# Kernel tuning notes

Hardware: AMD Instinct MI355X
Metric: run time of the kernel (lower is better)

The kernel has to match this reference:

```python
import jax, jax.numpy as jnp
import numpy as np

D_MODEL = 1024


def setup_inputs() -> dict:
    key = jax.random.key(0)
    ks = jax.random.split(key, 7)
    d = D_MODEL
    x = jax.random.normal(ks[0], (4, 2048, d), dtype=jnp.float32)
    scale = 1.0 / np.sqrt(d)
    Wq = jax.random.normal(ks[1], (d, d), dtype=jnp.float32) * scale
    bq = jax.random.normal(ks[2], (d,), dtype=jnp.float32) * 0.01
    Wk = jax.random.normal(ks[3], (d, d), dtype=jnp.float32) * scale
    bk = jax.random.normal(ks[4], (d,), dtype=jnp.float32) * 0.01
    Wo = jax.random.normal(ks[5], (d, 1), dtype=jnp.float32) * scale
    bo = jax.random.normal(ks[6], (1,), dtype=jnp.float32) * 0.01
    return {"x": x, "Wq": Wq, "bq": bq, "Wk": Wk, "bk": bk, "Wo": Wo, "bo": bo}


def reference(x, Wq, bq, Wk, bk, Wo, bo):
    # x: [B, N, d]
    Q = x @ Wq + bq                      # [B, N, d]
    K = x @ Wk + bk                      # [B, N, d]
    scale = x.shape[-1] ** (-0.5)
    content_logits = jnp.einsum('bnd,bmd->bnm', Q, K) * scale  # [B, N, N]
    s = (x @ Wo + bo)[..., 0]            # [B, N]
    # ordering_bias[b, i, j] = tanh(s[b, j] - s[b, i]) * 5
    ordering_bias = jnp.tanh(s[:, None, :] - s[:, :, None]) * 5.0
    return content_logits + ordering_bias
```

## Files before the change

kernel.cpp:

```cpp
#include <hip/hip_runtime.h>
#include <math.h>

#define D_MODEL 1024
#define SEQ 2048
#define SCALE 0.03125f

using bf16x8 = __attribute__((ext_vector_type(8))) short;
using f32x4  = __attribute__((ext_vector_type(4))) float;

__device__ __forceinline__ unsigned short f2bf(float f) {
  union { float f; unsigned int u; } v; v.f = f;
  return (unsigned short)((v.u + 0x7fffu + ((v.u >> 16) & 1u)) >> 16);
}

__device__ __forceinline__ void async_cp16(const void* g, void* l) {
  __builtin_amdgcn_global_load_lds(
      (const __attribute__((address_space(1))) void*)g,
      (__attribute__((address_space(3))) void*)l, 16, 0, 0);
}


__device__ __forceinline__ const unsigned short* sptr(
    const unsigned short* base, int row0, int t) {
  const int rr = t >> 3;
  const int ck = (t & 7) ^ (rr & 7);
  return base + (size_t)(row0 + rr) * D_MODEL + ck * 8;
}

#define STG8(KT, BUF) {                                                    \
    const unsigned short* a_ = sA + (KT) * 64;                             \
    const unsigned short* b_ = sB + (KT) * 64;                             \
    unsigned short* da_ = As + (BUF) * 8192 + t * 8;                       \
    unsigned short* db_ = Bs + (BUF) * 8192 + t * 8;                       \
    async_cp16(a_,                 da_);                                   \
    async_cp16(a_ + 32 * D_MODEL,  da_ + 2048);                            \
    async_cp16(a_ + 64 * D_MODEL,  da_ + 4096);                            \
    async_cp16(a_ + 96 * D_MODEL,  da_ + 6144);                            \
    async_cp16(b_,                 db_);                                   \
    async_cp16(b_ + 32 * D_MODEL,  db_ + 2048);                            \
    async_cp16(b_ + 64 * D_MODEL,  db_ + 4096);                            \
    async_cp16(b_ + 96 * D_MODEL,  db_ + 6144);                            \
  }

__device__ __forceinline__ void gemm128_bk64(
    const unsigned short* sA, const unsigned short* sB,
    unsigned short* As, unsigned short* Bs, int t, f32x4 acc[4][4]) {
  const int lane = t & 63, w = t >> 6;
  const int wm = w >> 1, wn = w & 1;
  const int l16 = lane & 15, quad = lane >> 4, x7 = l16 & 7;
  const int c0 = (quad ^ x7) * 8, c1 = ((4 | quad) ^ x7) * 8;

  STG8(0, 0);
  __syncthreads();

  #pragma unroll 2
  for (int kk = 0; kk < 16; ++kk) {
    const int cur = (kk & 1) * 8192;
    if (kk < 15) STG8(kk + 1, (kk & 1) ^ 1);
    bf16x8 afr[4][2], bfr[4][2];
    #pragma unroll
    for (int mt = 0; mt < 4; mt++) {
      const int base = cur + (wm * 64 + mt * 16 + l16) * 64;
      afr[mt][0] = *(const bf16x8*)(As + base + c0);
      afr[mt][1] = *(const bf16x8*)(As + base + c1);
    }
    #pragma unroll
    for (int nt = 0; nt < 4; nt++) {
      const int base = cur + (wn * 64 + nt * 16 + l16) * 64;
      bfr[nt][0] = *(const bf16x8*)(Bs + base + c0);
      bfr[nt][1] = *(const bf16x8*)(Bs + base + c1);
    }
    #pragma unroll
    for (int ks = 0; ks < 2; ks++)
      #pragma unroll
      for (int mt = 0; mt < 4; mt++)
        #pragma unroll
        for (int nt = 0; nt < 4; nt++)
          acc[mt][nt] = __builtin_amdgcn_mfma_f32_16x16x32_bf16(
              afr[mt][ks], bfr[nt][ks], acc[mt][nt], 0, 0, 0);
    __syncthreads();
  }
}

__device__ __forceinline__ void store_c_bf16(f32x4 acc[4][4],
                                             unsigned short* C, int ldc,
                                             int m0, int n0, int tid) {
  const int lane = tid & 63, w = tid >> 6;
  const int wm = w >> 1, wn = w & 1;
  const int l16 = lane & 15, quad = lane >> 4;
  #pragma unroll
  for (int mt = 0; mt < 4; mt++) {
    #pragma unroll
    for (int r = 0; r < 4; r++) {
      const int row = m0 + wm * 64 + mt * 16 + quad * 4 + r;
      unsigned short* cp = C + (size_t)row * ldc + n0 + wn * 64 + l16;
      #pragma unroll
      for (int nt = 0; nt < 4; nt++) cp[nt * 16] = f2bf(acc[mt][nt][r]);
    }
  }
}

__global__ __launch_bounds__(256) void wcvt_kernel(
    const float* __restrict__ Wq, const float* __restrict__ Wk,
    const float* __restrict__ bq, const float* __restrict__ bk,
    unsigned short* __restrict__ Wqb, unsigned short* __restrict__ Wkb,
    float* __restrict__ u, float* __restrict__ v, float* __restrict__ sc) {
  const int blk = blockIdx.x, tid = threadIdx.x;
  __shared__ float red[4];
  float p;
  if (blk < 2048) {
    const bool isq = blk < 1024;
    const int row = blk & 1023;
    const float* W = isq ? Wq : Wk;
    const float* bias = isq ? bk : bq;
    const float4 wv = ((const float4*)(W + (size_t)row * D_MODEL))[tid];
    const float4 bv = ((const float4*)bias)[tid];
    ushort4 o;
    o.x = f2bf(wv.x); o.y = f2bf(wv.y); o.z = f2bf(wv.z); o.w = f2bf(wv.w);
    ((ushort4*)((isq ? Wqb : Wkb) + (size_t)row * D_MODEL))[tid] = o;
    p = wv.x * bv.x + wv.y * bv.y + wv.z * bv.z + wv.w * bv.w;
    #pragma unroll
    for (int off = 32; off > 0; off >>= 1) p += __shfl_down(p, off, 64);
    if ((tid & 63) == 0) red[tid >> 6] = p;
    __syncthreads();
    if (tid == 0) (isq ? u : v)[row] = red[0] + red[1] + red[2] + red[3];
  } else {
    const float4 a = ((const float4*)bq)[tid];
    const float4 b = ((const float4*)bk)[tid];
    p = a.x * b.x + a.y * b.y + a.z * b.z + a.w * b.w;
    #pragma unroll
    for (int off = 32; off > 0; off >>= 1) p += __shfl_down(p, off, 64);
    if ((tid & 63) == 0) red[tid >> 6] = p;
    __syncthreads();
    if (tid == 0) sc[0] = SCALE * (red[0] + red[1] + red[2] + red[3]);
  }
}

__global__ __launch_bounds__(256) void prep_x_kernel(
    const float* __restrict__ x, const float* __restrict__ Wo,
    const float* __restrict__ bo, const float* __restrict__ u,
    const float* __restrict__ v, const float* __restrict__ sc,
    unsigned short* __restrict__ xb, float* __restrict__ tb,
    float* __restrict__ aa, float* __restrict__ bb) {
  const int m = blockIdx.x, tid = threadIdx.x;
  const float4 xv = ((const float4*)(x + (size_t)m * D_MODEL))[tid];
  const float4 wv = ((const float4*)Wo)[tid];
  const float4 uv = ((const float4*)u)[tid];
  const float4 vv = ((const float4*)v)[tid];
  ushort4 o;
  o.x = f2bf(xv.x); o.y = f2bf(xv.y); o.z = f2bf(xv.z); o.w = f2bf(xv.w);
  ((ushort4*)(xb + (size_t)m * D_MODEL))[tid] = o;
  float p0 = xv.x * wv.x + xv.y * wv.y + xv.z * wv.z + xv.w * wv.w;
  float p1 = xv.x * uv.x + xv.y * uv.y + xv.z * uv.z + xv.w * uv.w;
  float p2 = xv.x * vv.x + xv.y * vv.y + xv.z * vv.z + xv.w * vv.w;
  #pragma unroll
  for (int off = 32; off > 0; off >>= 1) {
    p0 += __shfl_down(p0, off, 64);
    p1 += __shfl_down(p1, off, 64);
    p2 += __shfl_down(p2, off, 64);
  }
  __shared__ float red[3][4];
  if ((tid & 63) == 0) {
    red[0][tid >> 6] = p0; red[1][tid >> 6] = p1; red[2][tid >> 6] = p2;
  }
  __syncthreads();
  if (tid == 0) {
    tb[m] = tanhf(red[0][0] + red[0][1] + red[0][2] + red[0][3] + bo[0]);
    aa[m] = SCALE * (red[1][0] + red[1][1] + red[1][2] + red[1][3]) + sc[0];
    bb[m] = SCALE * (red[2][0] + red[2][1] + red[2][2] + red[2][3]);
  }
}

__global__ __launch_bounds__(256, 2) void wmm_kernel(
    const unsigned short* __restrict__ Wkb,
    const unsigned short* __restrict__ Wqb, unsigned short* __restrict__ Mt) {
  const int m0 = blockIdx.x * 128, n0 = blockIdx.y * 128;
  __shared__ unsigned short As[2 * 8192], Bs[2 * 8192];
  const int t = threadIdx.x;
  f32x4 acc[4][4];
  #pragma unroll
  for (int i = 0; i < 4; i++)
    #pragma unroll
    for (int j = 0; j < 4; j++) acc[i][j] = f32x4{0.f, 0.f, 0.f, 0.f};
  gemm128_bk64(sptr(Wkb, m0, t), sptr(Wqb, n0, t), As, Bs, t, acc);
  store_c_bf16(acc, Mt, D_MODEL, m0, n0, t);
}

__global__ __launch_bounds__(256, 2) void zgen_kernel(
    const unsigned short* __restrict__ xb,
    const unsigned short* __restrict__ Mt, unsigned short* __restrict__ Zb) {
  const int m0 = blockIdx.x * 128, n0 = blockIdx.y * 128;
  __shared__ unsigned short As[2 * 8192], Bs[2 * 8192];
  const int t = threadIdx.x;
  f32x4 acc[4][4];
  #pragma unroll
  for (int i = 0; i < 4; i++)
    #pragma unroll
    for (int j = 0; j < 4; j++) acc[i][j] = f32x4{0.f, 0.f, 0.f, 0.f};
  gemm128_bk64(sptr(xb, m0, t), sptr(Mt, n0, t), As, Bs, t, acc);
  store_c_bf16(acc, Zb, D_MODEL, m0, n0, t);
}

__global__ __launch_bounds__(256, 2) void zxt_kernel(
    const unsigned short* __restrict__ Zb, const unsigned short* __restrict__ xb,
    const float* __restrict__ tb, const float* __restrict__ aa,
    const float* __restrict__ bb, float* __restrict__ out) {
  __shared__ unsigned short As[2 * 8192], Bs[2 * 8192];
  __shared__ float tsi[128], tsa[128], tsj[128], tsb2[128];
  const int n = blockIdx.z * 256 + blockIdx.y * 16 + blockIdx.x;
  const int xcd = n & 7, q = n >> 3;
  const int b = q >> 5, r = q & 31;
  const int i0 = ((xcd >> 1) * 4 + (r >> 3)) * 128;
  const int j0 = ((xcd & 1) * 8 + (r & 7)) * 128;
  const int t = threadIdx.x;

  if (t < 128) {
    tsi[t] = tb[b * SEQ + i0 + t];
    tsa[t] = aa[b * SEQ + i0 + t];
  } else {
    tsj[t - 128] = tb[b * SEQ + j0 + t - 128];
    tsb2[t - 128] = bb[b * SEQ + j0 + t - 128];
  }

  f32x4 acc[4][4];
  #pragma unroll
  for (int i = 0; i < 4; i++)
    #pragma unroll
    for (int j = 0; j < 4; j++) acc[i][j] = f32x4{0.f, 0.f, 0.f, 0.f};
  gemm128_bk64(sptr(Zb + (size_t)b * SEQ * D_MODEL, i0, t),
               sptr(xb + (size_t)b * SEQ * D_MODEL, j0, t), As, Bs, t, acc);

  const int lane = t & 63, w = t >> 6;
  const int wm = w >> 1, wn = w & 1;
  const int l16 = lane & 15, quad = lane >> 4;
  float tj[4], bj[4];
  #pragma unroll
  for (int nt = 0; nt < 4; nt++) {
    tj[nt] = tsj[wn * 64 + nt * 16 + l16];
    bj[nt] = tsb2[wn * 64 + nt * 16 + l16];
  }
  #pragma unroll
  for (int mt = 0; mt < 4; mt++) {
    #pragma unroll
    for (int rr = 0; rr < 4; rr++) {
      const int il = wm * 64 + mt * 16 + quad * 4 + rr;
      const float ti = tsi[il];
      const float ai = tsa[il];
      float* cp =
          out + ((size_t)(b * SEQ + i0 + il)) * SEQ + j0 + wn * 64 + l16;
      #pragma unroll
      for (int nt = 0; nt < 4; nt++) {
        const float num = tj[nt] - ti;
        const float den = fmaf(-tj[nt], ti, 1.0f);
        const float obias = 5.0f * num * __builtin_amdgcn_rcpf(den);
        cp[nt * 16] = SCALE * acc[mt][nt][rr] + ai + bj[nt] + obias;
      }
    }
  }
}

extern "C" void kernel_launch(void* const* d_in, const int* in_sizes, int n_in,
                              void* d_out, int out_size, void* d_ws,
                              size_t ws_size, hipStream_t stream) {
  const float* x  = (const float*)d_in[0];
  const float* Wq = (const float*)d_in[1];
  const float* bq = (const float*)d_in[2];
  const float* Wk = (const float*)d_in[3];
  const float* bk = (const float*)d_in[4];
  const float* Wo = (const float*)d_in[5];
  const float* bo = (const float*)d_in[6];
  float* out = (float*)d_out;

  char* ws = (char*)d_ws;
  unsigned short* xb  = (unsigned short*)(ws);
  unsigned short* Zb  = (unsigned short*)(ws + (16ull << 20));
  unsigned short* Wqb = (unsigned short*)(ws + (32ull << 20));
  unsigned short* Wkb = (unsigned short*)(ws + (34ull << 20));
  unsigned short* Mt  = (unsigned short*)(ws + (36ull << 20));
  float* tb = (float*)(ws + (38ull << 20));
  float* aa = (float*)(ws + (38ull << 20) + (32ull << 10));
  float* bb = (float*)(ws + (38ull << 20) + (64ull << 10));
  float* u  = (float*)(ws + (38ull << 20) + (96ull << 10));
  float* v  = (float*)(ws + (38ull << 20) + (100ull << 10));
  float* sc = (float*)(ws + (38ull << 20) + (104ull << 10));

  wcvt_kernel<<<2049, 256, 0, stream>>>(Wq, Wk, bq, bk, Wqb, Wkb, u, v, sc);
  prep_x_kernel<<<8192, 256, 0, stream>>>(x, Wo, bo, u, v, sc, xb, tb, aa, bb);
  wmm_kernel<<<dim3(8, 8), 256, 0, stream>>>(Wkb, Wqb, Mt);
  zgen_kernel<<<dim3(64, 8), 256, 0, stream>>>(xb, Mt, Zb);
  zxt_kernel<<<dim3(16, 16, 4), 256, 0, stream>>>(Zb, xb, tb, aa, bb, out);
}
```

Before: 182.7 us.

## Fuse all stages into one persistent kernel with grid-wide barriers

Replaces the five separate launches with a single persistent 512-block kernel that runs every stage and separates dependent stages with atomic-counter grid barriers. The weight-product GEMM (Wk·Wq) now overlaps with the x-conversion stage by giving those tiles to blocks 448-511 while the other blocks convert x. This removes launch gaps and tail idle time between small kernels. In exchange it depends on all 512 blocks being co-resident (two per CU), adds spin-wait barrier cost, and puts all x-conversion work on fewer blocks.

```diff
diff --git a/kernel.cpp b/kernel.cpp
--- a/kernel.cpp
+++ b/kernel.cpp
@@ -4,6 +4,7 @@
 #define D_MODEL 1024
 #define SEQ 2048
 #define SCALE 0.03125f
+#define NBLK 512u
 
 using bf16x8 = __attribute__((ext_vector_type(8))) short;
 using f32x4  = __attribute__((ext_vector_type(4))) float;
@@ -17,6 +18,20 @@
   __builtin_amdgcn_global_load_lds(
       (const __attribute__((address_space(1))) void*)g,
       (__attribute__((address_space(3))) void*)l, 16, 0, 0);
+}
+
+__device__ __forceinline__ void grid_barrier(unsigned int* cnt) {
+  __syncthreads();
+  if (threadIdx.x == 0) {
+    __threadfence();
+    __hip_atomic_fetch_add(cnt, 1u, __ATOMIC_ACQ_REL, __HIP_MEMORY_SCOPE_AGENT);
+    while (__hip_atomic_load(cnt, __ATOMIC_ACQUIRE, __HIP_MEMORY_SCOPE_AGENT) <
+           NBLK) {
+      __builtin_amdgcn_s_sleep(8);
+    }
+    __threadfence();
+  }
+  __syncthreads();
 }
 
 
@@ -100,160 +115,162 @@
   }
 }
 
-__global__ __launch_bounds__(256) void wcvt_kernel(
-    const float* __restrict__ Wq, const float* __restrict__ Wk,
-    const float* __restrict__ bq, const float* __restrict__ bk,
+__global__ __launch_bounds__(256, 2) void mega_kernel(
+    const float* __restrict__ x, const float* __restrict__ Wq,
+    const float* __restrict__ bq, const float* __restrict__ Wk,
+    const float* __restrict__ bk, const float* __restrict__ Wo,
+    const float* __restrict__ bo, float* __restrict__ out,
+    unsigned short* __restrict__ xb, unsigned short* __restrict__ Zb,
     unsigned short* __restrict__ Wqb, unsigned short* __restrict__ Wkb,
-    float* __restrict__ u, float* __restrict__ v, float* __restrict__ sc) {
-  const int blk = blockIdx.x, tid = threadIdx.x;
-  __shared__ float red[4];
-  float p;
-  if (blk < 2048) {
-    const bool isq = blk < 1024;
-    const int row = blk & 1023;
-    const float* W = isq ? Wq : Wk;
-    const float* bias = isq ? bk : bq;
-    const float4 wv = ((const float4*)(W + (size_t)row * D_MODEL))[tid];
-    const float4 bv = ((const float4*)bias)[tid];
-    ushort4 o;
-    o.x = f2bf(wv.x); o.y = f2bf(wv.y); o.z = f2bf(wv.z); o.w = f2bf(wv.w);
-    ((ushort4*)((isq ? Wqb : Wkb) + (size_t)row * D_MODEL))[tid] = o;
-    p = wv.x * bv.x + wv.y * bv.y + wv.z * bv.z + wv.w * bv.w;
-    #pragma unroll
-    for (int off = 32; off > 0; off >>= 1) p += __shfl_down(p, off, 64);
-    if ((tid & 63) == 0) red[tid >> 6] = p;
-    __syncthreads();
-    if (tid == 0) (isq ? u : v)[row] = red[0] + red[1] + red[2] + red[3];
+    unsigned short* __restrict__ Mt, float* __restrict__ tb,
+    float* __restrict__ aa, float* __restrict__ bb, float* __restrict__ u,
+    float* __restrict__ v, float* __restrict__ sc,
+    unsigned int* __restrict__ bar) {
+  __shared__ unsigned short As[2 * 8192], Bs[2 * 8192];
+  __shared__ float bias4[4][128];
+  __shared__ float red3[3][4];
+  const int blk = blockIdx.x, t = threadIdx.x;
+
+  for (int item = blk; item < 2049; item += 512) {
+    float p;
+    if (item < 2048) {
+      const bool isq = item < 1024;
+      const int row = item & 1023;
+      const float* W = isq ? Wq : Wk;
+      const float* bias = isq ? bk : bq;
+      const float4 wv = ((const float4*)(W + (size_t)row * D_MODEL))[t];
+      const float4 bv = ((const float4*)bias)[t];
+      ushort4 o;
+      o.x = f2bf(wv.x); o.y = f2bf(wv.y); o.z = f2bf(wv.z); o.w = f2bf(wv.w);
+      ((ushort4*)((isq ? Wqb : Wkb) + (size_t)row * D_MODEL))[t] = o;
+      p = wv.x * bv.x + wv.y * bv.y + wv.z * bv.z + wv.w * bv.w;
+      #pragma unroll
+      for (int off = 32; off > 0; off >>= 1) p += __shfl_down(p, off, 64);
+      if ((t & 63) == 0) red3[0][t >> 6] = p;
+      __syncthreads();
+      if (t == 0)
+        (isq ? u : v)[row] = red3[0][0] + red3[0][1] + red3[0][2] + red3[0][3];
+      __syncthreads();
+    } else {
+      const float4 a = ((const float4*)bq)[t];
+      const float4 b = ((const float4*)bk)[t];
+      p = a.x * b.x + a.y * b.y + a.z * b.z + a.w * b.w;
+      #pragma unroll
+      for (int off = 32; off > 0; off >>= 1) p += __shfl_down(p, off, 64);
+      if ((t & 63) == 0) red3[0][t >> 6] = p;
+      __syncthreads();
+      if (t == 0)
+        sc[0] = SCALE * (red3[0][0] + red3[0][1] + red3[0][2] + red3[0][3]);
+      __syncthreads();
+    }
+  }
+  grid_barrier(bar + 0);
+
+  if (blk < 448) {
+    const float4 wv = ((const float4*)Wo)[t];
+    const float4 uv = ((const float4*)u)[t];
+    const float4 vv = ((const float4*)v)[t];
+    const float scv = sc[0];
+    const float bov = bo[0];
+    for (int m = blk; m < 8192; m += 448) {
+      const float4 xv = ((const float4*)(x + (size_t)m * D_MODEL))[t];
+      ushort4 o;
+      o.x = f2bf(xv.x); o.y = f2bf(xv.y); o.z = f2bf(xv.z); o.w = f2bf(xv.w);
+      ((ushort4*)(xb + (size_t)m * D_MODEL))[t] = o;
+      float p0 = xv.x * wv.x + xv.y * wv.y + xv.z * wv.z + xv.w * wv.w;
+      float p1 = xv.x * uv.x + xv.y * uv.y + xv.z * uv.z + xv.w * uv.w;
+      float p2 = xv.x * vv.x + xv.y * vv.y + xv.z * vv.z + xv.w * vv.w;
+      #pragma unroll
+      for (int off = 32; off > 0; off >>= 1) {
+        p0 += __shfl_down(p0, off, 64);
+        p1 += __shfl_down(p1, off, 64);
+        p2 += __shfl_down(p2, off, 64);
+      }
+      if ((t & 63) == 0) {
+        red3[0][t >> 6] = p0; red3[1][t >> 6] = p1; red3[2][t >> 6] = p2;
+      }
+      __syncthreads();
+      if (t == 0) {
+        tb[m] = tanhf(red3[0][0] + red3[0][1] + red3[0][2] + red3[0][3] + bov);
+        aa[m] = SCALE * (red3[1][0] + red3[1][1] + red3[1][2] + red3[1][3]) + scv;
+        bb[m] = SCALE * (red3[2][0] + red3[2][1] + red3[2][2] + red3[2][3]);
+      }
+      __syncthreads();
+    }
   } else {
-    const float4 a = ((const float4*)bq)[tid];
-    const float4 b = ((const float4*)bk)[tid];
-    p = a.x * b.x + a.y * b.y + a.z * b.z + a.w * b.w;
-    #pragma unroll
-    for (int off = 32; off > 0; off >>= 1) p += __shfl_down(p, off, 64);
-    if ((tid & 63) == 0) red[tid >> 6] = p;
-    __syncthreads();
-    if (tid == 0) sc[0] = SCALE * (red[0] + red[1] + red[2] + red[3]);
-  }
-}
-
-__global__ __launch_bounds__(256) void prep_x_kernel(
-    const float* __restrict__ x, const float* __restrict__ Wo,
-    const float* __restrict__ bo, const float* __restrict__ u,
-    const float* __restrict__ v, const float* __restrict__ sc,
-    unsigned short* __restrict__ xb, float* __restrict__ tb,
-    float* __restrict__ aa, float* __restrict__ bb) {
-  const int m = blockIdx.x, tid = threadIdx.x;
-  const float4 xv = ((const float4*)(x + (size_t)m * D_MODEL))[tid];
-  const float4 wv = ((const float4*)Wo)[tid];
-  const float4 uv = ((const float4*)u)[tid];
-  const float4 vv = ((const float4*)v)[tid];
-  ushort4 o;
-  o.x = f2bf(xv.x); o.y = f2bf(xv.y); o.z = f2bf(xv.z); o.w = f2bf(xv.w);
-  ((ushort4*)(xb + (size_t)m * D_MODEL))[tid] = o;
-  float p0 = xv.x * wv.x + xv.y * wv.y + xv.z * wv.z + xv.w * wv.w;
-  float p1 = xv.x * uv.x + xv.y * uv.y + xv.z * uv.z + xv.w * uv.w;
-  float p2 = xv.x * vv.x + xv.y * vv.y + xv.z * vv.z + xv.w * vv.w;
-  #pragma unroll
-  for (int off = 32; off > 0; off >>= 1) {
-    p0 += __shfl_down(p0, off, 64);
-    p1 += __shfl_down(p1, off, 64);
-    p2 += __shfl_down(p2, off, 64);
-  }
-  __shared__ float red[3][4];
-  if ((tid & 63) == 0) {
-    red[0][tid >> 6] = p0; red[1][tid >> 6] = p1; red[2][tid >> 6] = p2;
-  }
-  __syncthreads();
-  if (tid == 0) {
-    tb[m] = tanhf(red[0][0] + red[0][1] + red[0][2] + red[0][3] + bo[0]);
-    aa[m] = SCALE * (red[1][0] + red[1][1] + red[1][2] + red[1][3]) + sc[0];
-    bb[m] = SCALE * (red[2][0] + red[2][1] + red[2][2] + red[2][3]);
-  }
-}
-
-__global__ __launch_bounds__(256, 2) void wmm_kernel(
-    const unsigned short* __restrict__ Wkb,
-    const unsigned short* __restrict__ Wqb, unsigned short* __restrict__ Mt) {
-  const int m0 = blockIdx.x * 128, n0 = blockIdx.y * 128;
-  __shared__ unsigned short As[2 * 8192], Bs[2 * 8192];
-  const int t = threadIdx.x;
-  f32x4 acc[4][4];
-  #pragma unroll
-  for (int i = 0; i < 4; i++)
-    #pragma unroll
-    for (int j = 0; j < 4; j++) acc[i][j] = f32x4{0.f, 0.f, 0.f, 0.f};
-  gemm128_bk64(sptr(Wkb, m0, t), sptr(Wqb, n0, t), As, Bs, t, acc);
-  store_c_bf16(acc, Mt, D_MODEL, m0, n0, t);
-}
-
-__global__ __launch_bounds__(256, 2) void zgen_kernel(
-    const unsigned short* __restrict__ xb,
-    const unsigned short* __restrict__ Mt, unsigned short* __restrict__ Zb) {
-  const int m0 = blockIdx.x * 128, n0 = blockIdx.y * 128;
-  __shared__ unsigned short As[2 * 8192], Bs[2 * 8192];
-  const int t = threadIdx.x;
-  f32x4 acc[4][4];
-  #pragma unroll
-  for (int i = 0; i < 4; i++)
-    #pragma unroll
-    for (int j = 0; j < 4; j++) acc[i][j] = f32x4{0.f, 0.f, 0.f, 0.f};
-  gemm128_bk64(sptr(xb, m0, t), sptr(Mt, n0, t), As, Bs, t, acc);
-  store_c_bf16(acc, Zb, D_MODEL, m0, n0, t);
-}
-
-__global__ __launch_bounds__(256, 2) void zxt_kernel(
-    const unsigned short* __restrict__ Zb, const unsigned short* __restrict__ xb,
-    const float* __restrict__ tb, const float* __restrict__ aa,
-    const float* __restrict__ bb, float* __restrict__ out) {
-  __shared__ unsigned short As[2 * 8192], Bs[2 * 8192];
-  __shared__ float tsi[128], tsa[128], tsj[128], tsb2[128];
-  const int n = blockIdx.z * 256 + blockIdx.y * 16 + blockIdx.x;
-  const int xcd = n & 7, q = n >> 3;
-  const int b = q >> 5, r = q & 31;
-  const int i0 = ((xcd >> 1) * 4 + (r >> 3)) * 128;
-  const int j0 = ((xcd & 1) * 8 + (r & 7)) * 128;
-  const int t = threadIdx.x;
-
-  if (t < 128) {
-    tsi[t] = tb[b * SEQ + i0 + t];
-    tsa[t] = aa[b * SEQ + i0 + t];
-  } else {
-    tsj[t - 128] = tb[b * SEQ + j0 + t - 128];
-    tsb2[t - 128] = bb[b * SEQ + j0 + t - 128];
-  }
-
-  f32x4 acc[4][4];
-  #pragma unroll
-  for (int i = 0; i < 4; i++)
-    #pragma unroll
-    for (int j = 0; j < 4; j++) acc[i][j] = f32x4{0.f, 0.f, 0.f, 0.f};
-  gemm128_bk64(sptr(Zb + (size_t)b * SEQ * D_MODEL, i0, t),
-               sptr(xb + (size_t)b * SEQ * D_MODEL, j0, t), As, Bs, t, acc);
+    const int tile = blk - 448;
+    const int m0 = (tile & 7) * 128, n0 = (tile >> 3) * 128;
+    f32x4 acc[4][4];
+    #pragma unroll
+    for (int i = 0; i < 4; i++)
+      #pragma unroll
+      for (int j = 0; j < 4; j++) acc[i][j] = f32x4{0.f, 0.f, 0.f, 0.f};
+    gemm128_bk64(sptr(Wkb, m0, t), sptr(Wqb, n0, t), As, Bs, t, acc);
+    store_c_bf16(acc, Mt, D_MODEL, m0, n0, t);
+  }
+  grid_barrier(bar + 32);
+
+  {
+    const int xcd = blk & 7, q = blk >> 3;
+    const int m0 = (xcd * 8 + (q & 7)) * 128;
+    const int n0 = (q >> 3) * 128;
+    f32x4 acc[4][4];
+    #pragma unroll
+    for (int i = 0; i < 4; i++)
+      #pragma unroll
+      for (int j = 0; j < 4; j++) acc[i][j] = f32x4{0.f, 0.f, 0.f, 0.f};
+    gemm128_bk64(sptr(xb, m0, t), sptr(Mt, n0, t), As, Bs, t, acc);
+    store_c_bf16(acc, Zb, D_MODEL, m0, n0, t);
+  }
+  grid_barrier(bar + 64);
 
   const int lane = t & 63, w = t >> 6;
   const int wm = w >> 1, wn = w & 1;
   const int l16 = lane & 15, quad = lane >> 4;
-  float tj[4], bj[4];
-  #pragma unroll
-  for (int nt = 0; nt < 4; nt++) {
-    tj[nt] = tsj[wn * 64 + nt * 16 + l16];
-    bj[nt] = tsb2[wn * 64 + nt * 16 + l16];
-  }
-  #pragma unroll
-  for (int mt = 0; mt < 4; mt++) {
-    #pragma unroll
-    for (int rr = 0; rr < 4; rr++) {
-      const int il = wm * 64 + mt * 16 + quad * 4 + rr;
-      const float ti = tsi[il];
-      const float ai = tsa[il];
-      float* cp =
-          out + ((size_t)(b * SEQ + i0 + il)) * SEQ + j0 + wn * 64 + l16;
-      #pragma unroll
-      for (int nt = 0; nt < 4; nt++) {
-        const float num = tj[nt] - ti;
-        const float den = fmaf(-tj[nt], ti, 1.0f);
-        const float obias = 5.0f * num * __builtin_amdgcn_rcpf(den);
-        cp[nt * 16] = SCALE * acc[mt][nt][rr] + ai + bj[nt] + obias;
+  for (int it = 0; it < 2; ++it) {
+    const int n = blk + 512 * it;
+    const int xcd = n & 7, q = n >> 3;
+    const int b = q >> 5, r = q & 31;
+    const int i0 = ((xcd >> 1) * 4 + (r >> 3)) * 128;
+    const int j0 = ((xcd & 1) * 8 + (r & 7)) * 128;
+    __syncthreads();
+    if (t < 128) {
+      bias4[0][t] = tb[b * SEQ + i0 + t];
+      bias4[1][t] = aa[b * SEQ + i0 + t];
+    } else {
+      bias4[2][t - 128] = tb[b * SEQ + j0 + t - 128];
+      bias4[3][t - 128] = bb[b * SEQ + j0 + t - 128];
+    }
+    f32x4 acc[4][4];
+    #pragma unroll
+    for (int i = 0; i < 4; i++)
+      #pragma unroll
+      for (int j = 0; j < 4; j++) acc[i][j] = f32x4{0.f, 0.f, 0.f, 0.f};
+    gemm128_bk64(sptr(Zb + (size_t)b * SEQ * D_MODEL, i0, t),
+                 sptr(xb + (size_t)b * SEQ * D_MODEL, j0, t), As, Bs, t, acc);
+
+    float tj[4], bj[4];
+    #pragma unroll
+    for (int nt = 0; nt < 4; nt++) {
+      tj[nt] = bias4[2][wn * 64 + nt * 16 + l16];
+      bj[nt] = bias4[3][wn * 64 + nt * 16 + l16];
+    }
+    #pragma unroll
+    for (int mt = 0; mt < 4; mt++) {
+      #pragma unroll
+      for (int rr = 0; rr < 4; rr++) {
+        const int il = wm * 64 + mt * 16 + quad * 4 + rr;
+        const float ti = bias4[0][il];
+        const float ai = bias4[1][il];
+        float* cp =
+            out + ((size_t)(b * SEQ + i0 + il)) * SEQ + j0 + wn * 64 + l16;
+        #pragma unroll
+        for (int nt = 0; nt < 4; nt++) {
+          const float num = tj[nt] - ti;
+          const float den = fmaf(-tj[nt], ti, 1.0f);
+          const float obias = 5.0f * num * __builtin_amdgcn_rcpf(den);
+          cp[nt * 16] = SCALE * acc[mt][nt][rr] + ai + bj[nt] + obias;
+        }
       }
     }
   }
@@ -283,10 +300,10 @@
   float* u  = (float*)(ws + (38ull << 20) + (96ull << 10));
   float* v  = (float*)(ws + (38ull << 20) + (100ull << 10));
   float* sc = (float*)(ws + (38ull << 20) + (104ull << 10));
-
-  wcvt_kernel<<<2049, 256, 0, stream>>>(Wq, Wk, bq, bk, Wqb, Wkb, u, v, sc);
-  prep_x_kernel<<<8192, 256, 0, stream>>>(x, Wo, bo, u, v, sc, xb, tb, aa, bb);
-  wmm_kernel<<<dim3(8, 8), 256, 0, stream>>>(Wkb, Wqb, Mt);
-  zgen_kernel<<<dim3(64, 8), 256, 0, stream>>>(xb, Mt, Zb);
-  zxt_kernel<<<dim3(16, 16, 4), 256, 0, stream>>>(Zb, xb, tb, aa, bb, out);
-}
+  unsigned int* bar = (unsigned int*)(ws + (38ull << 20) + (112ull << 10));
+
+  hipMemsetAsync(bar, 0, 512, stream);
+  mega_kernel<<<NBLK, 256, 0, stream>>>(x, Wq, bq, Wk, bk, Wo, bo, out, xb, Zb,
+                                        Wqb, Wkb, Mt, tb, aa, bb, u, v, sc,
+                                        bar);
+}
```

Result: slower. 373.0 us (+104.1%).

## Triple-buffer BK32 pipeline in zxt kernel and XCD-aware tile mapping for zgen

Applied to the files above, without the earlier changes.

The main output GEMM kernel now has its own inline main loop with K-tiles of 32, a three-stage LDS ring buffer and async global-to-LDS copies issued two tiles ahead, gated by vmcnt waits. Smaller LDS use lets occupancy rise from 2 to 3 blocks per CU. The per-row and per-column bias and tanh tables are read straight from global memory instead of being staged in shared memory. Separately, zgen remaps block IDs so that neighbouring tiles land on the same XCD for better L2 reuse. The trade-off is more barriers per unit of K and scattered scalar global loads in the epilogue.

```diff
diff --git a/kernel.cpp b/kernel.cpp
--- a/kernel.cpp
+++ b/kernel.cpp
@@ -189,7 +189,10 @@
 __global__ __launch_bounds__(256, 2) void zgen_kernel(
     const unsigned short* __restrict__ xb,
     const unsigned short* __restrict__ Mt, unsigned short* __restrict__ Zb) {
-  const int m0 = blockIdx.x * 128, n0 = blockIdx.y * 128;
+  const int id = blockIdx.y * 64 + blockIdx.x;
+  const int xcd = id & 7, q = id >> 3;
+  const int m0 = (xcd * 8 + (q & 7)) * 128;
+  const int n0 = (q >> 3) * 128;
   __shared__ unsigned short As[2 * 8192], Bs[2 * 8192];
   const int t = threadIdx.x;
   f32x4 acc[4][4];
@@ -201,51 +204,97 @@
   store_c_bf16(acc, Zb, D_MODEL, m0, n0, t);
 }
 
-__global__ __launch_bounds__(256, 2) void zxt_kernel(
+__global__ __launch_bounds__(256, 3) void zxt_kernel(
     const unsigned short* __restrict__ Zb, const unsigned short* __restrict__ xb,
     const float* __restrict__ tb, const float* __restrict__ aa,
     const float* __restrict__ bb, float* __restrict__ out) {
-  __shared__ unsigned short As[2 * 8192], Bs[2 * 8192];
-  __shared__ float tsi[128], tsa[128], tsj[128], tsb2[128];
+  __shared__ unsigned short As[3 * 4096], Bs[3 * 4096];
   const int n = blockIdx.z * 256 + blockIdx.y * 16 + blockIdx.x;
   const int xcd = n & 7, q = n >> 3;
   const int b = q >> 5, r = q & 31;
   const int i0 = ((xcd >> 1) * 4 + (r >> 3)) * 128;
   const int j0 = ((xcd & 1) * 8 + (r & 7)) * 128;
   const int t = threadIdx.x;
-
-  if (t < 128) {
-    tsi[t] = tb[b * SEQ + i0 + t];
-    tsa[t] = aa[b * SEQ + i0 + t];
-  } else {
-    tsj[t - 128] = tb[b * SEQ + j0 + t - 128];
-    tsb2[t - 128] = bb[b * SEQ + j0 + t - 128];
-  }
-
-  f32x4 acc[4][4];
-  #pragma unroll
-  for (int i = 0; i < 4; i++)
-    #pragma unroll
-    for (int j = 0; j < 4; j++) acc[i][j] = f32x4{0.f, 0.f, 0.f, 0.f};
-  gemm128_bk64(sptr(Zb + (size_t)b * SEQ * D_MODEL, i0, t),
-               sptr(xb + (size_t)b * SEQ * D_MODEL, j0, t), As, Bs, t, acc);
-
   const int lane = t & 63, w = t >> 6;
   const int wm = w >> 1, wn = w & 1;
   const int l16 = lane & 15, quad = lane >> 4;
+  const int ck8 = (quad ^ (l16 & 3)) * 8;
+
+  const int srow = t >> 2;
+  const int sc_ = (t & 3) ^ (srow & 3);
+  const unsigned short* sA =
+      Zb + ((size_t)b * SEQ + i0 + srow) * D_MODEL + sc_ * 8;
+  const unsigned short* sB =
+      xb + ((size_t)b * SEQ + j0 + srow) * D_MODEL + sc_ * 8;
+
+  #define STG4(KT, BUFO) {                                        \
+      async_cp16(sA + (KT) * 32,         As + (BUFO) + t * 8);    \
+      async_cp16(sA + 65536 + (KT) * 32, As + (BUFO) + 2048 + t * 8); \
+      async_cp16(sB + (KT) * 32,         Bs + (BUFO) + t * 8);    \
+      async_cp16(sB + 65536 + (KT) * 32, Bs + (BUFO) + 2048 + t * 8); }
+
+  f32x4 acc[4][4];
+  #pragma unroll
+  for (int i = 0; i < 4; i++)
+    #pragma unroll
+    for (int j = 0; j < 4; j++) acc[i][j] = f32x4{0.f, 0.f, 0.f, 0.f};
+
+  STG4(0, 0);
+  STG4(1, 4096);
+
+  int cur = 0, stg = 8192;
+  #pragma unroll 3
+  for (int kk = 0; kk < 31; ++kk) {
+    asm volatile("s_waitcnt vmcnt(4)" ::: "memory");
+    __builtin_amdgcn_s_barrier();
+    if (kk < 30) STG4(kk + 2, stg);
+    bf16x8 afr[4], bfr[4];
+    #pragma unroll
+    for (int mt = 0; mt < 4; mt++)
+      afr[mt] = *(const bf16x8*)(As + cur + (wm * 64 + mt * 16 + l16) * 32 + ck8);
+    #pragma unroll
+    for (int nt = 0; nt < 4; nt++)
+      bfr[nt] = *(const bf16x8*)(Bs + cur + (wn * 64 + nt * 16 + l16) * 32 + ck8);
+    #pragma unroll
+    for (int mt = 0; mt < 4; mt++)
+      #pragma unroll
+      for (int nt = 0; nt < 4; nt++)
+        acc[mt][nt] = __builtin_amdgcn_mfma_f32_16x16x32_bf16(
+            afr[mt], bfr[nt], acc[mt][nt], 0, 0, 0);
+    cur = (cur == 8192) ? 0 : cur + 4096;
+    stg = (stg == 8192) ? 0 : stg + 4096;
+  }
+  asm volatile("s_waitcnt vmcnt(0)" ::: "memory");
+  __builtin_amdgcn_s_barrier();
+  {
+    bf16x8 afr[4], bfr[4];
+    #pragma unroll
+    for (int mt = 0; mt < 4; mt++)
+      afr[mt] = *(const bf16x8*)(As + cur + (wm * 64 + mt * 16 + l16) * 32 + ck8);
+    #pragma unroll
+    for (int nt = 0; nt < 4; nt++)
+      bfr[nt] = *(const bf16x8*)(Bs + cur + (wn * 64 + nt * 16 + l16) * 32 + ck8);
+    #pragma unroll
+    for (int mt = 0; mt < 4; mt++)
+      #pragma unroll
+      for (int nt = 0; nt < 4; nt++)
+        acc[mt][nt] = __builtin_amdgcn_mfma_f32_16x16x32_bf16(
+            afr[mt], bfr[nt], acc[mt][nt], 0, 0, 0);
+  }
+
   float tj[4], bj[4];
   #pragma unroll
   for (int nt = 0; nt < 4; nt++) {
-    tj[nt] = tsj[wn * 64 + nt * 16 + l16];
-    bj[nt] = tsb2[wn * 64 + nt * 16 + l16];
+    tj[nt] = tb[b * SEQ + j0 + wn * 64 + nt * 16 + l16];
+    bj[nt] = bb[b * SEQ + j0 + wn * 64 + nt * 16 + l16];
   }
   #pragma unroll
   for (int mt = 0; mt < 4; mt++) {
     #pragma unroll
     for (int rr = 0; rr < 4; rr++) {
       const int il = wm * 64 + mt * 16 + quad * 4 + rr;
-      const float ti = tsi[il];
-      const float ai = tsa[il];
+      const float ti = tb[b * SEQ + i0 + il];
+      const float ai = aa[b * SEQ + i0 + il];
       float* cp =
           out + ((size_t)(b * SEQ + i0 + il)) * SEQ + j0 + wn * 64 + l16;
       #pragma unroll
```

Measured after the change: 187.4 us. 2.6% more time.
